# Kernel tuning notes

Measured on AMD Instinct MI355X. Metric: run time of the kernel, lower is better.

The kernel has to match this reference:

```python
import jax, jax.numpy as jnp
import numpy as np

FREQ = 10000.0

def absolute_position_bias(T, d):
    # AP[pos, 2i]   = sin(pos / freq**(2i/d))
    # AP[pos, 2i+1] = cos(pos / freq**(2i/d)), i in [0, T//2)
    pos = jnp.arange(T, dtype=jnp.float32)[:, None]          # [T,1]
    i = jnp.arange(T // 2, dtype=jnp.float32)[None, :]       # [1,T//2]
    angle = pos / (FREQ ** (2.0 * i / d))                    # [T,T//2]
    return jnp.stack([jnp.sin(angle), jnp.cos(angle)], axis=-1).reshape(T, T)

def setup_inputs() -> dict:
    key = jax.random.key(0)
    ks = jax.random.split(key, 5)
    T, D, H = 2048, 1024, 16
    dh = D // H
    s = 1.0 / np.sqrt(D)
    return {
        "x": jax.random.normal(ks[0], (T, D), dtype=jnp.float32),
        "Wq": jax.random.normal(ks[1], (H, D, dh), dtype=jnp.float32) * s,
        "Wk": jax.random.normal(ks[2], (H, D, dh), dtype=jnp.float32) * s,
        "Wv": jax.random.normal(ks[3], (H, D, dh), dtype=jnp.float32) * s,
        "Wout": jax.random.normal(ks[4], (D, D), dtype=jnp.float32) * s,
    }

def reference(x, Wq, Wk, Wv, Wout):
    T, D = x.shape
    H, _, dh = Wq.shape
    AP = absolute_position_bias(T, D)                        # [T,T]
    Q = jnp.einsum('td,hdk->htk', x, Wq)                     # [H,T,dh]
    K = jnp.einsum('td,hdk->htk', x, Wk)
    V = jnp.einsum('td,hdk->htk', x, Wv)
    scores = jnp.einsum('htk,hsk->hts', Q, K) + AP[None]     # [H,T,T] (no 1/sqrt(dk) scaling, faithful to source)
    attn = jax.nn.softmax(scores, axis=-1)                   # dropout omitted (eval mode)
    y = jnp.einsum('hts,hsk->htk', attn, V)                  # [H,T,dh]
    y = jnp.transpose(y, (1, 0, 2)).reshape(T, H * dh)       # concat heads along features
    y = y @ Wout.T                                           # out Linear, bias=False
    return y, attn[-1]  # source returns last head's attention weights
```

## Files before the change

kernel.cpp:

```cpp
#include <hip/hip_runtime.h>
#include <math.h>

constexpr int T  = 2048;
constexpr int Dm = 1024;
constexpr int NH = 16;
constexpr int DH = 64;
constexpr int KS = 4;

typedef unsigned short u16;
typedef _Float16 f16;
typedef f16 f16x8 __attribute__((ext_vector_type(8)));
typedef __fp16 fp16x2 __attribute__((ext_vector_type(2)));
typedef float f32x4 __attribute__((ext_vector_type(4)));

#define MFMAH(a, b, c) __builtin_amdgcn_mfma_f32_16x16x32_f16((a), (b), (c), 0, 0, 0)

__device__ __forceinline__ float h2f(u16 h) {
    union { u16 u; f16 h; } v; v.u = h; return (float)v.h;
}
__device__ __forceinline__ u16 f2h(float f) {
    union { u16 u; f16 h; } v; v.h = (f16)f; return v.u;
}

__global__ __launch_bounds__(256) void invfreq_kernel(float* __restrict__ invfreq) {
    int c = blockIdx.x * 256 + threadIdx.x;
    if (c < T) {
        float e = (float)(c & ~1) / (float)Dm;
        invfreq[c] = powf(10000.0f, -e);
    }
}

__global__ __launch_bounds__(256) void ap_kernel(const float* __restrict__ invfreq,
                                                 u16* __restrict__ ap) {
    int p = blockIdx.x * 256 + threadIdx.x;
    int t = blockIdx.y;
    int s = p * 2;
    float f = invfreq[s];
    float sn, cs;
    __sincosf((float)t * f, &sn, &cs);
    unsigned int packed = (unsigned int)f2h(sn) | ((unsigned int)f2h(cs) << 16);
    *(unsigned int*)(ap + (size_t)t * T + s) = packed;
}

__global__ __launch_bounds__(256) void xconv_kernel(const float* __restrict__ x,
                                                    u16* __restrict__ xh) {
    size_t i = ((size_t)blockIdx.x * 256 + threadIdx.x) * 4;
    float4 v = *(const float4*)(x + i);
    ushort4 hv;
    hv.x = f2h(v.x); hv.y = f2h(v.y); hv.z = f2h(v.z); hv.w = f2h(v.w);
    *(ushort4*)(xh + i) = hv;
}

__global__ __launch_bounds__(256) void wtrans_kernel(
    const float* __restrict__ Wq, const float* __restrict__ Wk,
    const float* __restrict__ Wv, u16* __restrict__ Wt)
{
    const int z = blockIdx.z;
    const float* W = (z == 0) ? Wq : (z == 1) ? Wk : Wv;
    const int h = blockIdx.y, kc = blockIdx.x * 64;
    const int tid = threadIdx.x;

    __shared__ float Ls[64][65];
    #pragma unroll
    for (int it = 0; it < 4; ++it) {
        int idx = it * 256 + tid;
        int kl = idx >> 4, n4 = (idx & 15) * 4;
        float4 v = *(const float4*)(W + ((size_t)h * Dm + kc + kl) * DH + n4);
        Ls[n4+0][kl] = v.x; Ls[n4+1][kl] = v.y; Ls[n4+2][kl] = v.z; Ls[n4+3][kl] = v.w;
    }
    __syncthreads();

    const int n = tid >> 2, k16 = (tid & 3) * 16;
    union { u16 u[16]; int4 v[2]; } tmp;
    #pragma unroll
    for (int j = 0; j < 16; ++j) tmp.u[j] = f2h(Ls[n][k16 + j]);
    u16* dst = Wt + (((size_t)z * NH + h) * DH + n) * Dm + kc + k16;
    *(int4*)(dst)     = tmp.v[0];
    *(int4*)(dst + 8) = tmp.v[1];
}

__global__ __launch_bounds__(256) void wout_conv_kernel(const float* __restrict__ W,
                                                        u16* __restrict__ Wb) {
    size_t i = ((size_t)blockIdx.x * 256 + threadIdx.x) * 4;
    float4 v = *(const float4*)(W + i);
    ushort4 hv;
    hv.x = f2h(v.x); hv.y = f2h(v.y); hv.z = f2h(v.z); hv.w = f2h(v.w);
    *(ushort4*)(Wb + i) = hv;
}

__global__ __launch_bounds__(256) void proj_mfma(
    const u16* __restrict__ xh, const u16* __restrict__ Wt,
    u16* __restrict__ Qh, u16* __restrict__ Kh, u16* __restrict__ Vt)
{
    __shared__ u16 Xs[4096];
    __shared__ u16 WsQ[4096];
    __shared__ u16 WsK[4096];
    __shared__ u16 WsV[4096];

    const int t0 = blockIdx.x * 64, h = blockIdx.y;
    const int tid = threadIdx.x, w = tid >> 6, lane = tid & 63;
    const int b = lane & 15, a = lane >> 4;

    const int srow = tid >> 2, sc16 = (tid & 3) * 16;
    const int swz = (srow & 7) << 4;
    const int sb0 = (srow * 128 + sc16 * 2) ^ swz;
    const int sb1 = (srow * 128 + sc16 * 2 + 16) ^ swz;

    const u16* WQb = Wt + ((size_t)0 * NH + h) * DH * Dm;
    const u16* WKb = Wt + ((size_t)1 * NH + h) * DH * Dm;
    const u16* WVb = Wt + ((size_t)2 * NH + h) * DH * Dm;

    f32x4 aq[4], ak[4], av[4];
    #pragma unroll
    for (int ct = 0; ct < 4; ++ct) {
        aq[ct] = (f32x4){0.f, 0.f, 0.f, 0.f};
        ak[ct] = (f32x4){0.f, 0.f, 0.f, 0.f};
        av[ct] = (f32x4){0.f, 0.f, 0.f, 0.f};
    }

    for (int kc = 0; kc < Dm; kc += 64) {
        __syncthreads();
        {
            const u16* gx  = xh  + (size_t)(t0 + srow) * Dm + kc + sc16;
            const u16* gwq = WQb + (size_t)srow * Dm + kc + sc16;
            const u16* gwk = WKb + (size_t)srow * Dm + kc + sc16;
            const u16* gwv = WVb + (size_t)srow * Dm + kc + sc16;
            *(int4*)((char*)Xs  + sb0) = *(const int4*)gx;
            *(int4*)((char*)Xs  + sb1) = *(const int4*)(gx + 8);
            *(int4*)((char*)WsQ + sb0) = *(const int4*)gwq;
            *(int4*)((char*)WsQ + sb1) = *(const int4*)(gwq + 8);
            *(int4*)((char*)WsK + sb0) = *(const int4*)gwk;
            *(int4*)((char*)WsK + sb1) = *(const int4*)(gwk + 8);
            *(int4*)((char*)WsV + sb0) = *(const int4*)gwv;
            *(int4*)((char*)WsV + sb1) = *(const int4*)(gwv + 8);
        }
        __syncthreads();

        f16x8 ax[2];
        #pragma unroll
        for (int ks = 0; ks < 2; ++ks) {
            int row = 16 * w + b;
            int byt = (row * 128 + ks * 64 + a * 16) ^ ((row & 7) << 4);
            ax[ks] = *(const f16x8*)((const char*)Xs + byt);
        }
        __builtin_amdgcn_s_setprio(1);
        #pragma unroll
        for (int ct = 0; ct < 4; ++ct) {
            #pragma unroll
            for (int ks = 0; ks < 2; ++ks) {
                int row = 16 * ct + b;
                int byt = (row * 128 + ks * 64 + a * 16) ^ ((row & 7) << 4);
                f16x8 bq = *(const f16x8*)((const char*)WsQ + byt);
                f16x8 bk = *(const f16x8*)((const char*)WsK + byt);
                f16x8 bv = *(const f16x8*)((const char*)WsV + byt);
                aq[ct] = MFMAH(ax[ks], bq, aq[ct]);
                ak[ct] = MFMAH(ax[ks], bk, ak[ct]);
                av[ct] = MFMAH(ax[ks], bv, av[ct]);
            }
        }
        __builtin_amdgcn_s_setprio(0);
    }

    const size_t base = (size_t)h * T * DH;
    #pragma unroll
    for (int ct = 0; ct < 4; ++ct) {
        #pragma unroll
        for (int r = 0; r < 4; ++r) {
            int t = t0 + 16 * w + a * 4 + r;
            size_t off = base + (size_t)t * DH + 16 * ct + b;
            Qh[off] = f2h(aq[ct][r]);
            Kh[off] = f2h(ak[ct][r]);
            Vt[((size_t)h * DH + 16 * ct + b) * T + t] = f2h(av[ct][r]);
        }
    }
}

__global__ __launch_bounds__(256) void flash_mfma_split(
    const u16* __restrict__ Qh, const u16* __restrict__ Kh,
    const u16* __restrict__ Vt, const u16* __restrict__ AP,
    u16* __restrict__ Opart, float2* __restrict__ ml)
{
    __shared__ u16 Ks[4096];
    __shared__ u16 Vs[4096];
    __shared__ u16 Ps[4][1024];

    const int h = blockIdx.y, t0 = blockIdx.x * 64;
    const int split = blockIdx.z;
    const int s_begin = split * (T / KS), s_end = s_begin + T / KS;
    const int tid = threadIdx.x, w = tid >> 6, lane = tid & 63;
    const int b = lane & 15, a = lane >> 4;

    const size_t hTD = (size_t)h * T * DH;
    const int trow = t0 + 16 * w + b;

    const size_t qoff = hTD + (size_t)trow * DH + a * 8;
    f16x8 qf[2];
    qf[0] = *(const f16x8*)(Qh + qoff);
    qf[1] = *(const f16x8*)(Qh + qoff + 32);

    f32x4 oacc[4];
    float m_run = -INFINITY, l_run = 0.f;
    #pragma unroll
    for (int i = 0; i < 4; ++i) oacc[i] = (f32x4){0.f, 0.f, 0.f, 0.f};

    const int srow = tid >> 2, sc16 = (tid & 3) * 16;
    const int swz = (srow & 7) << 4;
    const int sb0 = (srow * 128 + sc16 * 2) ^ swz;
    const int sb1 = (srow * 128 + sc16 * 2 + 16) ^ swz;

    const u16* aprow = AP + (size_t)trow * T;

    for (int s0 = s_begin; s0 < s_end; s0 += 64) {
        __syncthreads();
        {
            const u16* gk = Kh + hTD + (size_t)(s0 + srow) * DH + sc16;
            const u16* gv = Vt + hTD + (size_t)srow * T + s0 + sc16;
            *(int4*)((char*)Ks + sb0) = *(const int4*)gk;
            *(int4*)((char*)Ks + sb1) = *(const int4*)(gk + 8);
            *(int4*)((char*)Vs + sb0) = *(const int4*)gv;
            *(int4*)((char*)Vs + sb1) = *(const int4*)(gv + 8);
        }
        __syncthreads();

        ushort4 ap4[4];
        #pragma unroll
        for (int ct = 0; ct < 4; ++ct)
            ap4[ct] = *(const ushort4*)(aprow + s0 + 16 * ct + 4 * a);

        f32x4 acc[4];
        #pragma unroll
        for (int ct = 0; ct < 4; ++ct) acc[ct] = (f32x4){0.f, 0.f, 0.f, 0.f};
        #pragma unroll
        for (int ct = 0; ct < 4; ++ct) {
            #pragma unroll
            for (int ks = 0; ks < 2; ++ks) {
                int row = 16 * ct + b;
                int byt = (row * 128 + ks * 64 + a * 16) ^ ((row & 7) << 4);
                f16x8 kf = *(const f16x8*)((const char*)Ks + byt);
                acc[ct] = MFMAH(kf, qf[ks], acc[ct]);
            }
        }

        #pragma unroll
        for (int ct = 0; ct < 4; ++ct) {
            const u16* apu = (const u16*)&ap4[ct];
            #pragma unroll
            for (int r = 0; r < 4; ++r)
                acc[ct][r] += h2f(apu[r]);
        }

        float mx = acc[0][0];
        #pragma unroll
        for (int ct = 0; ct < 4; ++ct)
            #pragma unroll
            for (int r = 0; r < 4; ++r) mx = fmaxf(mx, acc[ct][r]);
        mx = fmaxf(mx, __shfl_xor(mx, 16));
        mx = fmaxf(mx, __shfl_xor(mx, 32));

        float mnew  = fmaxf(m_run, mx);
        float alpha = __expf(m_run - mnew);
        float rs = 0.f;
        #pragma unroll
        for (int ct = 0; ct < 4; ++ct) {
            #pragma unroll
            for (int r = 0; r < 4; ++r) {
                float p = __expf(acc[ct][r] - mnew);
                acc[ct][r] = p;
                rs += p;
            }
        }
        rs += __shfl_xor(rs, 16);
        rs += __shfl_xor(rs, 32);
        l_run = l_run * alpha + rs;
        m_run = mnew;
        #pragma unroll
        for (int dt = 0; dt < 4; ++dt) {
            oacc[dt][0] *= alpha; oacc[dt][1] *= alpha;
            oacc[dt][2] *= alpha; oacc[dt][3] *= alpha;
        }

        #pragma unroll
        for (int ct = 0; ct < 4; ++ct) {
            union { fp16x2 h[2]; int2 i2; } u;
            u.h[0] = __builtin_amdgcn_cvt_pkrtz(acc[ct][0], acc[ct][1]);
            u.h[1] = __builtin_amdgcn_cvt_pkrtz(acc[ct][2], acc[ct][3]);
            int byt = (b * 128 + ct * 32 + a * 8) ^ ((b & 7) << 4);
            *(int2*)((char*)Ps[w] + byt) = u.i2;
        }

        f16x8 pa[2];
        #pragma unroll
        for (int ks = 0; ks < 2; ++ks) {
            int byt = (b * 128 + ks * 64 + a * 16) ^ ((b & 7) << 4);
            pa[ks] = *(const f16x8*)((const char*)Ps[w] + byt);
        }
        #pragma unroll
        for (int dt = 0; dt < 4; ++dt) {
            #pragma unroll
            for (int ks = 0; ks < 2; ++ks) {
                int row = 16 * dt + b;
                int byt = (row * 128 + ks * 64 + a * 16) ^ ((row & 7) << 4);
                f16x8 vf = *(const f16x8*)((const char*)Vs + byt);
                oacc[dt] = MFMAH(vf, pa[ks], oacc[dt]);
            }
        }
    }

    const size_t pbase = ((size_t)split * NH + h) * T;
    #pragma unroll
    for (int dt = 0; dt < 4; ++dt) {
        ushort4 ov;
        ov.x = f2h(oacc[dt][0]); ov.y = f2h(oacc[dt][1]);
        ov.z = f2h(oacc[dt][2]); ov.w = f2h(oacc[dt][3]);
        *(ushort4*)(Opart + (pbase + trow) * DH + 16 * dt + 4 * a) = ov;
    }
    if (a == 0) ml[pbase + trow] = make_float2(m_run, l_run);
}

__global__ __launch_bounds__(256) void flash_combine(
    const u16* __restrict__ Opart, const float2* __restrict__ ml,
    u16* __restrict__ Ych, float2* __restrict__ mlfinal)
{
    int idx = blockIdx.x * 256 + threadIdx.x;
    int h = idx >> 14;
    int rem = idx & 16383;
    int t = rem >> 3;
    int d8 = (rem & 7) * 8;

    float2 mls[KS];
    size_t rr[KS];
    float m = -INFINITY;
    #pragma unroll
    for (int s = 0; s < KS; ++s) {
        rr[s] = ((size_t)s * NH + h) * T + t;
        mls[s] = ml[rr[s]];
        m = fmaxf(m, mls[s].x);
    }
    float wgt[KS], L = 0.f;
    #pragma unroll
    for (int s = 0; s < KS; ++s) {
        wgt[s] = __expf(mls[s].x - m);
        L += wgt[s] * mls[s].y;
    }
    float inv = 1.f / L;
    if (h == NH - 1 && d8 == 0) mlfinal[t] = make_float2(m, inv);

    float o[8] = {};
    #pragma unroll
    for (int s = 0; s < KS; ++s) {
        union { u16 u[8]; int4 v; } ov;
        ov.v = *(const int4*)(Opart + rr[s] * DH + d8);
        float ws = wgt[s] * inv;
        #pragma unroll
        for (int j = 0; j < 8; ++j) o[j] += h2f(ov.u[j]) * ws;
    }
    union { u16 u[8]; int4 v; } yo;
    #pragma unroll
    for (int j = 0; j < 8; ++j) yo.u[j] = f2h(o[j]);
    *(int4*)(Ych + (size_t)t * Dm + h * DH + d8) = yo.v;
}

__global__ __launch_bounds__(256) void score_mfma(
    const u16* __restrict__ Qh, const u16* __restrict__ Kh,
    const u16* __restrict__ AP, const float2* __restrict__ mlf,
    float* __restrict__ S)
{
    __shared__ u16 Ks[4096];

    const int h = NH - 1;
    const int s0 = blockIdx.x * 64, t0 = blockIdx.y * 64;
    const int tid = threadIdx.x, w = tid >> 6, lane = tid & 63;
    const int b = lane & 15, a = lane >> 4;
    const size_t hTD = (size_t)h * T * DH;
    const int trow = t0 + 16 * w + b;

    {
        const int srow = tid >> 2, sc16 = (tid & 3) * 16;
        const int swz = (srow & 7) << 4;
        const int sb0 = (srow * 128 + sc16 * 2) ^ swz;
        const int sb1 = (srow * 128 + sc16 * 2 + 16) ^ swz;
        const u16* gk = Kh + hTD + (size_t)(s0 + srow) * DH + sc16;
        *(int4*)((char*)Ks + sb0) = *(const int4*)gk;
        *(int4*)((char*)Ks + sb1) = *(const int4*)(gk + 8);
    }

    const size_t qoff = hTD + (size_t)trow * DH + a * 8;
    f16x8 qf[2];
    qf[0] = *(const f16x8*)(Qh + qoff);
    qf[1] = *(const f16x8*)(Qh + qoff + 32);
    __syncthreads();

    ushort4 ap4[4];
    #pragma unroll
    for (int ct = 0; ct < 4; ++ct)
        ap4[ct] = *(const ushort4*)(AP + (size_t)trow * T + s0 + 16 * ct + 4 * a);
    float2 fml = mlf[trow];

    f32x4 acc[4];
    #pragma unroll
    for (int ct = 0; ct < 4; ++ct) acc[ct] = (f32x4){0.f, 0.f, 0.f, 0.f};
    #pragma unroll
    for (int ct = 0; ct < 4; ++ct) {
        #pragma unroll
        for (int ks = 0; ks < 2; ++ks) {
            int row = 16 * ct + b;
            int byt = (row * 128 + ks * 64 + a * 16) ^ ((row & 7) << 4);
            f16x8 kf = *(const f16x8*)((const char*)Ks + byt);
            acc[ct] = MFMAH(kf, qf[ks], acc[ct]);
        }
    }

    #pragma unroll
    for (int ct = 0; ct < 4; ++ct) {
        const u16* apu = (const u16*)&ap4[ct];
        float4 o;
        o.x = __expf(acc[ct][0] + h2f(apu[0]) - fml.x) * fml.y;
        o.y = __expf(acc[ct][1] + h2f(apu[1]) - fml.x) * fml.y;
        o.z = __expf(acc[ct][2] + h2f(apu[2]) - fml.x) * fml.y;
        o.w = __expf(acc[ct][3] + h2f(apu[3]) - fml.x) * fml.y;
        *(float4*)(S + (size_t)trow * T + s0 + 16 * ct + 4 * a) = o;
    }
}

__global__ __launch_bounds__(256) void gemm_out_mfma(
    const u16* __restrict__ Ych, const u16* __restrict__ Wb,
    float* __restrict__ y)
{
    __shared__ u16 As[4096];
    __shared__ u16 Bs[4096];

    const int n0 = blockIdx.x * 64, t0 = blockIdx.y * 64;
    const int tid = threadIdx.x, w = tid >> 6, lane = tid & 63;
    const int b = lane & 15, a = lane >> 4;

    const int srow = tid >> 2, sc16 = (tid & 3) * 16;
    const int swz = (srow & 7) << 4;
    const int sb0 = (srow * 128 + sc16 * 2) ^ swz;
    const int sb1 = (srow * 128 + sc16 * 2 + 16) ^ swz;

    f32x4 acc[4];
    #pragma unroll
    for (int ct = 0; ct < 4; ++ct) acc[ct] = (f32x4){0.f, 0.f, 0.f, 0.f};

    for (int kc = 0; kc < Dm; kc += 64) {
        __syncthreads();
        {
            const u16* ga = Ych + (size_t)(t0 + srow) * Dm + kc + sc16;
            const u16* gb = Wb  + (size_t)(n0 + srow) * Dm + kc + sc16;
            *(int4*)((char*)As + sb0) = *(const int4*)ga;
            *(int4*)((char*)As + sb1) = *(const int4*)(ga + 8);
            *(int4*)((char*)Bs + sb0) = *(const int4*)gb;
            *(int4*)((char*)Bs + sb1) = *(const int4*)(gb + 8);
        }
        __syncthreads();

        f16x8 af[2];
        #pragma unroll
        for (int ks = 0; ks < 2; ++ks) {
            int row = 16 * w + b;
            int byt = (row * 128 + ks * 64 + a * 16) ^ ((row & 7) << 4);
            af[ks] = *(const f16x8*)((const char*)As + byt);
        }
        __builtin_amdgcn_s_setprio(1);
        #pragma unroll
        for (int ct = 0; ct < 4; ++ct) {
            #pragma unroll
            for (int ks = 0; ks < 2; ++ks) {
                int row = 16 * ct + b;
                int byt = (row * 128 + ks * 64 + a * 16) ^ ((row & 7) << 4);
                f16x8 bw = *(const f16x8*)((const char*)Bs + byt);
                acc[ct] = MFMAH(af[ks], bw, acc[ct]);
            }
        }
        __builtin_amdgcn_s_setprio(0);
    }

    #pragma unroll
    for (int r = 0; r < 4; ++r) {
        int t = t0 + 16 * w + a * 4 + r;
        #pragma unroll
        for (int ct = 0; ct < 4; ++ct)
            y[(size_t)t * Dm + n0 + 16 * ct + b] = acc[ct][r];
    }
}

extern "C" void kernel_launch(void* const* d_in, const int* in_sizes, int n_in,
                              void* d_out, int out_size, void* d_ws, size_t ws_size,
                              hipStream_t stream)
{
    const float* x    = (const float*)d_in[0];
    const float* Wq   = (const float*)d_in[1];
    const float* Wk   = (const float*)d_in[2];
    const float* Wv   = (const float*)d_in[3];
    const float* Wout = (const float*)d_in[4];

    float* out      = (float*)d_out;
    float* y_out    = out;
    float* attn_out = out + (long)T * Dm;

    char* ws = (char*)d_ws;
    const size_t MB = 1024 * 1024;
    float* invfreq = (float*)ws;
    u16* Qh = (u16*)(ws + 8192);
    u16* Kh = (u16*)(ws + 8192 + 4 * MB);
    u16* Vt = (u16*)(ws + 8192 + 8 * MB);
    char* C = ws + 8192 + 12 * MB;
    u16* xh  = (u16*)(C);
    u16* Wtb = (u16*)(C + 4 * MB);
    u16* APt   = (u16*)(C);
    u16* Ych   = (u16*)(C + 8 * MB);
    u16* Woutb = (u16*)(C + 12 * MB);
    float2* mlfinal = (float2*)(C + 14 * MB);
    float2* mlbuf   = (float2*)(C + 15 * MB);
    u16* Opart = (u16*)attn_out;
    (void)ws_size;

    invfreq_kernel<<<dim3(8), dim3(256), 0, stream>>>(invfreq);

    xconv_kernel<<<dim3((T * Dm / 4) / 256), dim3(256), 0, stream>>>(x, xh);
    wtrans_kernel<<<dim3(Dm / 64, NH, 3), dim3(256), 0, stream>>>(Wq, Wk, Wv, Wtb);

    proj_mfma<<<dim3(T / 64, NH), dim3(256), 0, stream>>>(xh, Wtb, Qh, Kh, Vt);

    ap_kernel<<<dim3(T / 512, T), dim3(256), 0, stream>>>(invfreq, APt);
    wout_conv_kernel<<<dim3((Dm * Dm / 4) / 256), dim3(256), 0, stream>>>(Wout, Woutb);

    flash_mfma_split<<<dim3(T / 64, NH, KS), dim3(256), 0, stream>>>(
        Qh, Kh, Vt, APt, Opart, mlbuf);
    flash_combine<<<dim3(NH * T * 8 / 256), dim3(256), 0, stream>>>(
        Opart, mlbuf, Ych, mlfinal);

    score_mfma<<<dim3(T / 64, T / 64), dim3(256), 0, stream>>>(
        Qh, Kh, APt, mlfinal, attn_out);

    gemm_out_mfma<<<dim3(Dm / 64, T / 64), dim3(256), 0, stream>>>(Ych, Woutb, y_out);
}
```

Baseline: 129.5 us.

## Merge prep kernels and tail kernels into single launches; halve flash split count

Four preprocessing kernels (x conversion, QKV weight transpose, Wout conversion, position-bias table) are merged into one launch, and the inverse frequency is computed inline with exp2f instead of through a separate table kernel. The score kernel and output GEMM are fused into one grid so both run concurrently. The flash-attention key split count drops from 4 to 2. The workspace layout is reorganised so the fused kernels do not alias each other. The aim is to cut launch overhead and idle tails between small kernels, at the cost of less split parallelism in the attention kernel.

Measured after the change: 104.4 us, median of 3. 19.4% less time.

```diff
diff --git a/kernel.cpp b/kernel.cpp
--- a/kernel.cpp
+++ b/kernel.cpp
@@ -5,7 +5,7 @@
 constexpr int Dm = 1024;
 constexpr int NH = 16;
 constexpr int DH = 64;
-constexpr int KS = 4;
+constexpr int KS = 2;
 
 typedef unsigned short u16;
 typedef _Float16 f16;
@@ -22,70 +22,60 @@
     union { u16 u; f16 h; } v; v.h = (f16)f; return v.u;
 }
 
-__global__ __launch_bounds__(256) void invfreq_kernel(float* __restrict__ invfreq) {
-    int c = blockIdx.x * 256 + threadIdx.x;
-    if (c < T) {
-        float e = (float)(c & ~1) / (float)Dm;
-        invfreq[c] = powf(10000.0f, -e);
-    }
-}
-
-__global__ __launch_bounds__(256) void ap_kernel(const float* __restrict__ invfreq,
-                                                 u16* __restrict__ ap) {
-    int p = blockIdx.x * 256 + threadIdx.x;
-    int t = blockIdx.y;
-    int s = p * 2;
-    float f = invfreq[s];
-    float sn, cs;
-    __sincosf((float)t * f, &sn, &cs);
-    unsigned int packed = (unsigned int)f2h(sn) | ((unsigned int)f2h(cs) << 16);
-    *(unsigned int*)(ap + (size_t)t * T + s) = packed;
-}
-
-__global__ __launch_bounds__(256) void xconv_kernel(const float* __restrict__ x,
-                                                    u16* __restrict__ xh) {
-    size_t i = ((size_t)blockIdx.x * 256 + threadIdx.x) * 4;
-    float4 v = *(const float4*)(x + i);
-    ushort4 hv;
-    hv.x = f2h(v.x); hv.y = f2h(v.y); hv.z = f2h(v.z); hv.w = f2h(v.w);
-    *(ushort4*)(xh + i) = hv;
-}
-
-__global__ __launch_bounds__(256) void wtrans_kernel(
+__global__ __launch_bounds__(256) void prep_kernel(
+    const float* __restrict__ x,
     const float* __restrict__ Wq, const float* __restrict__ Wk,
-    const float* __restrict__ Wv, u16* __restrict__ Wt)
+    const float* __restrict__ Wv, const float* __restrict__ Wout,
+    u16* __restrict__ xh, u16* __restrict__ Wt,
+    u16* __restrict__ Wb, u16* __restrict__ ap)
 {
-    const int z = blockIdx.z;
-    const float* W = (z == 0) ? Wq : (z == 1) ? Wk : Wv;
-    const int h = blockIdx.y, kc = blockIdx.x * 64;
-    const int tid = threadIdx.x;
-
     __shared__ float Ls[64][65];
-    #pragma unroll
-    for (int it = 0; it < 4; ++it) {
-        int idx = it * 256 + tid;
-        int kl = idx >> 4, n4 = (idx & 15) * 4;
-        float4 v = *(const float4*)(W + ((size_t)h * Dm + kc + kl) * DH + n4);
-        Ls[n4+0][kl] = v.x; Ls[n4+1][kl] = v.y; Ls[n4+2][kl] = v.z; Ls[n4+3][kl] = v.w;
-    }
-    __syncthreads();
-
-    const int n = tid >> 2, k16 = (tid & 3) * 16;
-    union { u16 u[16]; int4 v[2]; } tmp;
-    #pragma unroll
-    for (int j = 0; j < 16; ++j) tmp.u[j] = f2h(Ls[n][k16 + j]);
-    u16* dst = Wt + (((size_t)z * NH + h) * DH + n) * Dm + kc + k16;
-    *(int4*)(dst)     = tmp.v[0];
-    *(int4*)(dst + 8) = tmp.v[1];
-}
-
-__global__ __launch_bounds__(256) void wout_conv_kernel(const float* __restrict__ W,
-                                                        u16* __restrict__ Wb) {
-    size_t i = ((size_t)blockIdx.x * 256 + threadIdx.x) * 4;
-    float4 v = *(const float4*)(W + i);
-    ushort4 hv;
-    hv.x = f2h(v.x); hv.y = f2h(v.y); hv.z = f2h(v.z); hv.w = f2h(v.w);
-    *(ushort4*)(Wb + i) = hv;
+    const int blk = blockIdx.x, tid = threadIdx.x;
+
+    if (blk < 2048) {
+        size_t i = ((size_t)blk * 256 + tid) * 4;
+        float4 v = *(const float4*)(x + i);
+        ushort4 hv;
+        hv.x = f2h(v.x); hv.y = f2h(v.y); hv.z = f2h(v.z); hv.w = f2h(v.w);
+        *(ushort4*)(xh + i) = hv;
+    } else if (blk < 2816) {
+        int rel = blk - 2048;
+        int kc = (rel & 15) * 64, h = (rel >> 4) & 15, z = rel >> 8;
+        const float* W = (z == 0) ? Wq : (z == 1) ? Wk : Wv;
+        #pragma unroll
+        for (int it = 0; it < 4; ++it) {
+            int idx = it * 256 + tid;
+            int kl = idx >> 4, n4 = (idx & 15) * 4;
+            float4 v = *(const float4*)(W + ((size_t)h * Dm + kc + kl) * DH + n4);
+            Ls[n4+0][kl] = v.x; Ls[n4+1][kl] = v.y;
+            Ls[n4+2][kl] = v.z; Ls[n4+3][kl] = v.w;
+        }
+        __syncthreads();
+        const int n = tid >> 2, k16 = (tid & 3) * 16;
+        union { u16 u[16]; int4 v[2]; } tmp;
+        #pragma unroll
+        for (int j = 0; j < 16; ++j) tmp.u[j] = f2h(Ls[n][k16 + j]);
+        u16* dst = Wt + (((size_t)z * NH + h) * DH + n) * Dm + kc + k16;
+        *(int4*)(dst)     = tmp.v[0];
+        *(int4*)(dst + 8) = tmp.v[1];
+    } else if (blk < 3840) {
+        int rel = blk - 2816;
+        size_t i = ((size_t)rel * 256 + tid) * 4;
+        float4 v = *(const float4*)(Wout + i);
+        ushort4 hv;
+        hv.x = f2h(v.x); hv.y = f2h(v.y); hv.z = f2h(v.z); hv.w = f2h(v.w);
+        *(ushort4*)(Wb + i) = hv;
+    } else {
+        int rel = blk - 3840;
+        int p = (rel & 3) * 256 + tid;
+        int t = rel >> 2;
+        int s = p * 2;
+        float f = exp2f(-(float)s * 0.01297671165f);
+        float sn, cs;
+        __sincosf((float)t * f, &sn, &cs);
+        unsigned int packed = (unsigned int)f2h(sn) | ((unsigned int)f2h(cs) << 16);
+        *(unsigned int*)(ap + (size_t)t * T + s) = packed;
+    }
 }
 
 __global__ __launch_bounds__(256) void proj_mfma(
@@ -360,127 +350,120 @@
     *(int4*)(Ych + (size_t)t * Dm + h * DH + d8) = yo.v;
 }
 
-__global__ __launch_bounds__(256) void score_mfma(
+__global__ __launch_bounds__(256) void tail_kernel(
     const u16* __restrict__ Qh, const u16* __restrict__ Kh,
     const u16* __restrict__ AP, const float2* __restrict__ mlf,
-    float* __restrict__ S)
+    const u16* __restrict__ Ych, const u16* __restrict__ Wb,
+    float* __restrict__ S, float* __restrict__ y)
 {
-    __shared__ u16 Ks[4096];
-
-    const int h = NH - 1;
-    const int s0 = blockIdx.x * 64, t0 = blockIdx.y * 64;
-    const int tid = threadIdx.x, w = tid >> 6, lane = tid & 63;
+    __shared__ u16 lds[8192];
+    const int blk = blockIdx.x, tid = threadIdx.x;
+    const int w = tid >> 6, lane = tid & 63;
     const int b = lane & 15, a = lane >> 4;
-    const size_t hTD = (size_t)h * T * DH;
-    const int trow = t0 + 16 * w + b;
-
-    {
-        const int srow = tid >> 2, sc16 = (tid & 3) * 16;
-        const int swz = (srow & 7) << 4;
-        const int sb0 = (srow * 128 + sc16 * 2) ^ swz;
-        const int sb1 = (srow * 128 + sc16 * 2 + 16) ^ swz;
-        const u16* gk = Kh + hTD + (size_t)(s0 + srow) * DH + sc16;
-        *(int4*)((char*)Ks + sb0) = *(const int4*)gk;
-        *(int4*)((char*)Ks + sb1) = *(const int4*)(gk + 8);
-    }
-
-    const size_t qoff = hTD + (size_t)trow * DH + a * 8;
-    f16x8 qf[2];
-    qf[0] = *(const f16x8*)(Qh + qoff);
-    qf[1] = *(const f16x8*)(Qh + qoff + 32);
-    __syncthreads();
-
-    ushort4 ap4[4];
-    #pragma unroll
-    for (int ct = 0; ct < 4; ++ct)
-        ap4[ct] = *(const ushort4*)(AP + (size_t)trow * T + s0 + 16 * ct + 4 * a);
-    float2 fml = mlf[trow];
-
-    f32x4 acc[4];
-    #pragma unroll
-    for (int ct = 0; ct < 4; ++ct) acc[ct] = (f32x4){0.f, 0.f, 0.f, 0.f};
-    #pragma unroll
-    for (int ct = 0; ct < 4; ++ct) {
-        #pragma unroll
-        for (int ks = 0; ks < 2; ++ks) {
-            int row = 16 * ct + b;
-            int byt = (row * 128 + ks * 64 + a * 16) ^ ((row & 7) << 4);
-            f16x8 kf = *(const f16x8*)((const char*)Ks + byt);
-            acc[ct] = MFMAH(kf, qf[ks], acc[ct]);
-        }
-    }
-
-    #pragma unroll
-    for (int ct = 0; ct < 4; ++ct) {
-        const u16* apu = (const u16*)&ap4[ct];
-        float4 o;
-        o.x = __expf(acc[ct][0] + h2f(apu[0]) - fml.x) * fml.y;
-        o.y = __expf(acc[ct][1] + h2f(apu[1]) - fml.x) * fml.y;
-        o.z = __expf(acc[ct][2] + h2f(apu[2]) - fml.x) * fml.y;
-        o.w = __expf(acc[ct][3] + h2f(apu[3]) - fml.x) * fml.y;
-        *(float4*)(S + (size_t)trow * T + s0 + 16 * ct + 4 * a) = o;
-    }
-}
-
-__global__ __launch_bounds__(256) void gemm_out_mfma(
-    const u16* __restrict__ Ych, const u16* __restrict__ Wb,
-    float* __restrict__ y)
-{
-    __shared__ u16 As[4096];
-    __shared__ u16 Bs[4096];
-
-    const int n0 = blockIdx.x * 64, t0 = blockIdx.y * 64;
-    const int tid = threadIdx.x, w = tid >> 6, lane = tid & 63;
-    const int b = lane & 15, a = lane >> 4;
-
     const int srow = tid >> 2, sc16 = (tid & 3) * 16;
     const int swz = (srow & 7) << 4;
     const int sb0 = (srow * 128 + sc16 * 2) ^ swz;
     const int sb1 = (srow * 128 + sc16 * 2 + 16) ^ swz;
 
-    f32x4 acc[4];
-    #pragma unroll
-    for (int ct = 0; ct < 4; ++ct) acc[ct] = (f32x4){0.f, 0.f, 0.f, 0.f};
-
-    for (int kc = 0; kc < Dm; kc += 64) {
+    if (blk < 512) {
+        u16* As = lds;
+        u16* Bs = lds + 4096;
+        const int n0 = (blk & 15) * 64, t0 = (blk >> 4) * 64;
+
+        f32x4 acc[4];
+        #pragma unroll
+        for (int ct = 0; ct < 4; ++ct) acc[ct] = (f32x4){0.f, 0.f, 0.f, 0.f};
+
+        for (int kc = 0; kc < Dm; kc += 64) {
+            __syncthreads();
+            {
+                const u16* ga = Ych + (size_t)(t0 + srow) * Dm + kc + sc16;
+                const u16* gb = Wb  + (size_t)(n0 + srow) * Dm + kc + sc16;
+                *(int4*)((char*)As + sb0) = *(const int4*)ga;
+                *(int4*)((char*)As + sb1) = *(const int4*)(ga + 8);
+                *(int4*)((char*)Bs + sb0) = *(const int4*)gb;
+                *(int4*)((char*)Bs + sb1) = *(const int4*)(gb + 8);
+            }
+            __syncthreads();
+
+            f16x8 af[2];
+            #pragma unroll
+            for (int ks = 0; ks < 2; ++ks) {
+                int row = 16 * w + b;
+                int byt = (row * 128 + ks * 64 + a * 16) ^ ((row & 7) << 4);
+                af[ks] = *(const f16x8*)((const char*)As + byt);
+            }
+            __builtin_amdgcn_s_setprio(1);
+            #pragma unroll
+            for (int ct = 0; ct < 4; ++ct) {
+                #pragma unroll
+                for (int ks = 0; ks < 2; ++ks) {
+                    int row = 16 * ct + b;
+                    int byt = (row * 128 + ks * 64 + a * 16) ^ ((row & 7) << 4);
+                    f16x8 bw = *(const f16x8*)((const char*)Bs + byt);
+                    acc[ct] = MFMAH(af[ks], bw, acc[ct]);
+                }
+            }
+            __builtin_amdgcn_s_setprio(0);
+        }
+
+        #pragma unroll
+        for (int r = 0; r < 4; ++r) {
+            int t = t0 + 16 * w + a * 4 + r;
+            #pragma unroll
+            for (int ct = 0; ct < 4; ++ct)
+                y[(size_t)t * Dm + n0 + 16 * ct + b] = acc[ct][r];
+        }
+    } else {
+        u16* Ks = lds;
+        const int rel = blk - 512;
+        const int s0 = (rel & 31) * 64, t0 = (rel >> 5) * 64;
+        const int h = NH - 1;
+        const size_t hTD = (size_t)h * T * DH;
+        const int trow = t0 + 16 * w + b;
+
+        {
+            const u16* gk = Kh + hTD + (size_t)(s0 + srow) * DH + sc16;
+            *(int4*)((char*)Ks + sb0) = *(const int4*)gk;
+            *(int4*)((char*)Ks + sb1) = *(const int4*)(gk + 8);
+        }
+
+        const size_t qoff = hTD + (size_t)trow * DH + a * 8;
+        f16x8 qf[2];
+        qf[0] = *(const f16x8*)(Qh + qoff);
+        qf[1] = *(const f16x8*)(Qh + qoff + 32);
         __syncthreads();
-        {
-            const u16* ga = Ych + (size_t)(t0 + srow) * Dm + kc + sc16;
-            const u16* gb = Wb  + (size_t)(n0 + srow) * Dm + kc + sc16;
-            *(int4*)((char*)As + sb0) = *(const int4*)ga;
-            *(int4*)((char*)As + sb1) = *(const int4*)(ga + 8);
-            *(int4*)((char*)Bs + sb0) = *(const int4*)gb;
-            *(int4*)((char*)Bs + sb1) = *(const int4*)(gb + 8);
-        }
-        __syncthreads();
-
-        f16x8 af[2];
-        #pragma unroll
-        for (int ks = 0; ks < 2; ++ks) {
-            int row = 16 * w + b;
-            int byt = (row * 128 + ks * 64 + a * 16) ^ ((row & 7) << 4);
-            af[ks] = *(const f16x8*)((const char*)As + byt);
-        }
-        __builtin_amdgcn_s_setprio(1);
+
+        ushort4 ap4[4];
+        #pragma unroll
+        for (int ct = 0; ct < 4; ++ct)
+            ap4[ct] = *(const ushort4*)(AP + (size_t)trow * T + s0 + 16 * ct + 4 * a);
+        float2 fml = mlf[trow];
+
+        f32x4 acc[4];
+        #pragma unroll
+        for (int ct = 0; ct < 4; ++ct) acc[ct] = (f32x4){0.f, 0.f, 0.f, 0.f};
         #pragma unroll
         for (int ct = 0; ct < 4; ++ct) {
             #pragma unroll
             for (int ks = 0; ks < 2; ++ks) {
                 int row = 16 * ct + b;
                 int byt = (row * 128 + ks * 64 + a * 16) ^ ((row & 7) << 4);
-                f16x8 bw = *(const f16x8*)((const char*)Bs + byt);
-                acc[ct] = MFMAH(af[ks], bw, acc[ct]);
-            }
-        }
-        __builtin_amdgcn_s_setprio(0);
-    }
-
-    #pragma unroll
-    for (int r = 0; r < 4; ++r) {
-        int t = t0 + 16 * w + a * 4 + r;
-        #pragma unroll
-        for (int ct = 0; ct < 4; ++ct)
-            y[(size_t)t * Dm + n0 + 16 * ct + b] = acc[ct][r];
+                f16x8 kf = *(const f16x8*)((const char*)Ks + byt);
+                acc[ct] = MFMAH(kf, qf[ks], acc[ct]);
+            }
+        }
+
+        #pragma unroll
+        for (int ct = 0; ct < 4; ++ct) {
+            const u16* apu = (const u16*)&ap4[ct];
+            float4 o;
+            o.x = __expf(acc[ct][0] + h2f(apu[0]) - fml.x) * fml.y;
+            o.y = __expf(acc[ct][1] + h2f(apu[1]) - fml.x) * fml.y;
+            o.z = __expf(acc[ct][2] + h2f(apu[2]) - fml.x) * fml.y;
+            o.w = __expf(acc[ct][3] + h2f(apu[3]) - fml.x) * fml.y;
+            *(float4*)(S + (size_t)trow * T + s0 + 16 * ct + 4 * a) = o;
+        }
     }
 }
 
@@ -500,38 +483,31 @@
 
     char* ws = (char*)d_ws;
     const size_t MB = 1024 * 1024;
-    float* invfreq = (float*)ws;
-    u16* Qh = (u16*)(ws + 8192);
-    u16* Kh = (u16*)(ws + 8192 + 4 * MB);
-    u16* Vt = (u16*)(ws + 8192 + 8 * MB);
-    char* C = ws + 8192 + 12 * MB;
-    u16* xh  = (u16*)(C);
-    u16* Wtb = (u16*)(C + 4 * MB);
-    u16* APt   = (u16*)(C);
-    u16* Ych   = (u16*)(C + 8 * MB);
-    u16* Woutb = (u16*)(C + 12 * MB);
-    float2* mlfinal = (float2*)(C + 14 * MB);
-    float2* mlbuf   = (float2*)(C + 15 * MB);
+    u16* Qh = (u16*)ws;
+    u16* Kh = (u16*)(ws + 4 * MB);
+    u16* Vt = (u16*)(ws + 8 * MB);
+    char* C = ws + 12 * MB;
+    u16* xh    = (u16*)C;
+    u16* Ych   = (u16*)C;
+    u16* Wtb   = (u16*)(C + 4 * MB);
+    u16* Woutb = (u16*)(C + 10 * MB);
+    u16* APt   = (u16*)(C + 12 * MB);
+    float2* mlfinal = (float2*)(C + 20 * MB);
+    float2* mlbuf   = (float2*)(C + 20 * MB + 65536);
     u16* Opart = (u16*)attn_out;
     (void)ws_size;
 
-    invfreq_kernel<<<dim3(8), dim3(256), 0, stream>>>(invfreq);
-
-    xconv_kernel<<<dim3((T * Dm / 4) / 256), dim3(256), 0, stream>>>(x, xh);
-    wtrans_kernel<<<dim3(Dm / 64, NH, 3), dim3(256), 0, stream>>>(Wq, Wk, Wv, Wtb);
+    prep_kernel<<<dim3(12032), dim3(256), 0, stream>>>(
+        x, Wq, Wk, Wv, Wout, xh, Wtb, Woutb, APt);
 
     proj_mfma<<<dim3(T / 64, NH), dim3(256), 0, stream>>>(xh, Wtb, Qh, Kh, Vt);
-
-    ap_kernel<<<dim3(T / 512, T), dim3(256), 0, stream>>>(invfreq, APt);
-    wout_conv_kernel<<<dim3((Dm * Dm / 4) / 256), dim3(256), 0, stream>>>(Wout, Woutb);
 
     flash_mfma_split<<<dim3(T / 64, NH, KS), dim3(256), 0, stream>>>(
         Qh, Kh, Vt, APt, Opart, mlbuf);
+
     flash_combine<<<dim3(NH * T * 8 / 256), dim3(256), 0, stream>>>(
         Opart, mlbuf, Ych, mlfinal);
 
-    score_mfma<<<dim3(T / 64, T / 64), dim3(256), 0, stream>>>(
-        Qh, Kh, APt, mlfinal, attn_out);
-
-    gemm_out_mfma<<<dim3(Dm / 64, T / 64), dim3(256), 0, stream>>>(Ych, Woutb, y_out);
-}
+    tail_kernel<<<dim3(1536), dim3(256), 0, stream>>>(
+        Qh, Kh, APt, mlfinal, Ych, Woutb, attn_out, y_out);
+}
```
